# Performance work log

Measured on AMD Instinct MI355X. Metric: run time of the kernel, lower is better.

Reference implementation:

```python
import jax, jax.numpy as jnp
import numpy as np

B, T, V, D, P, DEP = 64, 32, 32000, 1024, 8, 4
TAU = 1.0
EPS = 1e-5


def setup_inputs() -> dict:
    key = jax.random.key(0)
    ks = jax.random.split(key, 9)
    s = 0.02
    x = jax.random.randint(ks[0], (B, T), 0, V)
    emb = jax.random.normal(ks[1], (V, D), jnp.float32) * s
    pos = jax.random.normal(ks[2], (T, D), jnp.float32) * s
    # primitive library: n_prims MLPs (Linear -> GELU -> Linear), stacked
    w1 = jax.random.normal(ks[3], (P, D, D), jnp.float32) * s
    b1 = jnp.zeros((P, D), jnp.float32)
    w2 = jax.random.normal(ks[4], (P, D, D), jnp.float32) * s
    b2 = jnp.zeros((P, D), jnp.float32)
    # one selector Linear(dim, n_prims) per depth
    sel_w = jax.random.normal(ks[5], (DEP, P, D), jnp.float32) * s
    sel_b = jnp.zeros((DEP, P), jnp.float32)
    ln_g = jnp.ones((D,), jnp.float32)
    ln_b = jnp.zeros((D,), jnp.float32)
    head_w = jax.random.normal(ks[6], (V, D), jnp.float32) * s
    # fixed gumbel noise (replaces torch's in-op sampling, kept deterministic)
    u = jax.random.uniform(ks[7], (DEP, B, P), jnp.float32, 1e-6, 1.0 - 1e-6)
    gumbel = -jnp.log(-jnp.log(u))
    return dict(x=x, emb=emb, pos=pos, w1=w1, b1=b1, w2=w2, b2=b2,
                sel_w=sel_w, sel_b=sel_b, ln_g=ln_g, ln_b=ln_b,
                head_w=head_w, gumbel=gumbel)


def reference(x, emb, pos, w1, b1, w2, b2, sel_w, sel_b, ln_g, ln_b, head_w, gumbel):
    h = emb[x] + pos[None, :x.shape[1], :]          # [B,T,D]
    div = jnp.float32(0.0)
    unif = jnp.float32(1.0 / P)
    for d in range(DEP):
        ctx = h.mean(axis=1)                         # [B,D]
        logits = ctx @ sel_w[d].T + sel_b[d]         # [B,P]
        weights = jax.nn.softmax((logits + gumbel[d]) / TAU, axis=-1)
        # all primitives over all tokens at once (grouped GEMM), no T loop
        u1 = jax.nn.gelu(jnp.einsum('btd,pde->btpe', h, w1) + b1, approximate=False)
        prim = jnp.einsum('btpe,pef->btpf', u1, w2) + b2   # [B,T,P,D]
        h = h + jnp.einsum('btpf,bp->btf', prim, weights)  # residual add
        avg = weights.mean(axis=0)                   # [P]
        # F.kl_div(avg.log(), uniform, reduction='sum')
        div = div + jnp.sum(unif * (jnp.log(unif) - jnp.log(avg)))
    mu = h.mean(-1, keepdims=True)
    var = ((h - mu) ** 2).mean(-1, keepdims=True)
    hn = (h - mu) * jax.lax.rsqrt(var + EPS) * ln_g + ln_b
    return hn @ head_w.T, div
```

## Files before the change

kernel.cpp:

```cpp
#include <hip/hip_runtime.h>
#include <hip/hip_bf16.h>
#include <math.h>

typedef __bf16 bf16x8 __attribute__((ext_vector_type(8)));
typedef float  f32x4  __attribute__((ext_vector_type(4)));

struct __align__(8) bf16x4s { __hip_bfloat16 a, b, c, d; };

__device__ __forceinline__ void gload_lds16(const void* g, void* l) {
  __builtin_amdgcn_global_load_lds(
      (const __attribute__((address_space(1))) void*)g,
      (__attribute__((address_space(3))) void*)l, 16, 0, 0);
}

__device__ __forceinline__ float fast_gelu(float v) {
  float s = 0.70710678118654752f * v;
  float a = fabsf(s);
  float t = __builtin_amdgcn_rcpf(fmaf(0.3275911f, a, 1.0f));
  float p = t * fmaf(t, fmaf(t, fmaf(t, fmaf(t, 1.061405429f, -1.453152027f),
                                     1.421413741f), -0.284496736f), 0.254829592f);
  float e = __expf(-a * a);
  float er = copysignf(fmaf(-p, e, 1.0f), s);
  return 0.5f * v * (1.0f + er);
}

#define BAR()   asm volatile("s_barrier" ::: "memory")
#define SB0()   __builtin_amdgcn_sched_barrier(0)
#define VMC(N)  do { asm volatile("s_waitcnt vmcnt(" #N ")" ::: "memory"); \
                     __builtin_amdgcn_sched_barrier(0); } while (0)
#define P1()    __builtin_amdgcn_s_setprio(1)
#define P0()    __builtin_amdgcn_s_setprio(0)

#define MQ(MB, NB, AV, BV)                                                    \
  do {                                                                        \
    _Pragma("unroll")                                                         \
    for (int mi_ = 0; mi_ < 4; ++mi_)                                         \
      _Pragma("unroll")                                                       \
      for (int nj_ = 0; nj_ < 2; ++nj_)                                       \
        _Pragma("unroll")                                                     \
        for (int kk_ = 0; kk_ < 2; ++kk_)                                     \
          acc[MB + mi_][NB + nj_] = __builtin_amdgcn_mfma_f32_16x16x32_bf16(  \
              AV[mi_][kk_], BV[nj_][kk_], acc[MB + mi_][NB + nj_], 0, 0, 0);  \
  } while (0)

template<int EPI>
__global__ __launch_bounds__(512, 2)
void gemm_nt(const __hip_bfloat16* __restrict__ A,
             const __hip_bfloat16* __restrict__ B,
             const int K, const int Kc, const int N,
             const float* __restrict__ p0,
             const float* __restrict__ p1,
             float* __restrict__ f32out,
             __hip_bfloat16* __restrict__ bfout)
{
  __shared__ __align__(16) __hip_bfloat16 lds[65536];

  const int tid = threadIdx.x;
  const int lane = tid & 63, wid = tid >> 6;
  const int l15 = lane & 15, l4 = lane >> 4;
  const int r8 = lane >> 3, blk = lane & 7;
  const int wm = wid >> 2, wn = wid & 3;

  const int nx = gridDim.x;
  const int flat = blockIdx.x + nx * blockIdx.y;
  const int q = (nx * gridDim.y) >> 3;
  const int nid = (flat & 7) * q + (flat >> 3);
  const long m0 = (long)(nid % nx) * 256;
  const long n0 = (long)(nid / nx) * 256;

  const int kbeg = blockIdx.z * Kc;
  const int nt = Kc / 64;

  f32x4 acc[8][4] = {};
  bf16x8 arE[4][2], arL[4][2], brE[2][2], brL[2][2];

  auto stageA = [&](int buf, int h, int k0) {
#pragma unroll
    for (int p2 = 0; p2 < 2; ++p2) {
      int ch = p2 * 16 + h * 8 + wid;
      int row = ch * 8 + r8;
      gload_lds16(A + (m0 + row) * (long)K + k0 + ((blk ^ r8) << 3),
                  lds + buf * 16384 + ch * 512);
    }
  };
  auto stageB = [&](int buf, int h, int k0) {
#pragma unroll
    for (int p2 = 0; p2 < 2; ++p2) {
      int ch = (p2 * 2 + (wid >> 2)) * 8 + h * 4 + (wid & 3);
      int row = ch * 8 + r8;
      gload_lds16(B + (n0 + row) * (long)K + k0 + ((blk ^ r8) << 3),
                  lds + 32768 + buf * 16384 + ch * 512);
    }
  };
  auto readAE = [&](int buf) {
    const __hip_bfloat16* pA = lds + buf * 16384;
#pragma unroll
    for (int mi = 0; mi < 4; ++mi)
#pragma unroll
      for (int kk = 0; kk < 2; ++kk) {
        int row = wm * 128 + mi * 16 + l15;
        arE[mi][kk] = *(const bf16x8*)(pA + row * 64 + (((kk * 4 + l4) ^ (row & 7)) << 3));
      }
  };
  auto readAL = [&](int buf) {
    const __hip_bfloat16* pA = lds + buf * 16384;
#pragma unroll
    for (int mi = 0; mi < 4; ++mi)
#pragma unroll
      for (int kk = 0; kk < 2; ++kk) {
        int row = wm * 128 + 64 + mi * 16 + l15;
        arL[mi][kk] = *(const bf16x8*)(pA + row * 64 + (((kk * 4 + l4) ^ (row & 7)) << 3));
      }
  };
  auto readBE = [&](int buf) {
    const __hip_bfloat16* pB = lds + 32768 + buf * 16384;
#pragma unroll
    for (int nj = 0; nj < 2; ++nj)
#pragma unroll
      for (int kk = 0; kk < 2; ++kk) {
        int row = wn * 64 + nj * 16 + l15;
        brE[nj][kk] = *(const bf16x8*)(pB + row * 64 + (((kk * 4 + l4) ^ (row & 7)) << 3));
      }
  };
  auto readBL = [&](int buf) {
    const __hip_bfloat16* pB = lds + 32768 + buf * 16384;
#pragma unroll
    for (int nj = 0; nj < 2; ++nj)
#pragma unroll
      for (int kk = 0; kk < 2; ++kk) {
        int row = wn * 64 + 32 + nj * 16 + l15;
        brL[nj][kk] = *(const bf16x8*)(pB + row * 64 + (((kk * 4 + l4) ^ (row & 7)) << 3));
      }
  };

  stageA(0, 0, kbeg);
  stageB(0, 0, kbeg);
  stageB(0, 1, kbeg);
  stageA(0, 1, kbeg);
  stageA(1, 0, kbeg + 64);
  stageB(1, 0, kbeg + 64);
  stageB(1, 1, kbeg + 64);
  VMC(8);
  BAR();
  readAE(0); readBE(0);

  for (int s = 0; s < nt - 2; ++s) {
    const int b = s & 1;
    const int k1 = kbeg + (s + 1) * 64, k2 = kbeg + (s + 2) * 64;
    readBL(b);
    stageA(b ^ 1, 1, k1);
    SB0();
    P1(); MQ(0, 0, arE, brE); P0();
    VMC(8); BAR();
    readAL(b);
    stageA(b, 0, k2);
    SB0();
    P1(); MQ(0, 2, arE, brL); P0();
    VMC(8); BAR();
    readAE(b ^ 1);
    stageB(b, 0, k2);
    SB0();
    P1(); MQ(4, 0, arL, brE); P0();
    VMC(8); BAR();
    readBE(b ^ 1);
    stageB(b, 1, k2);
    SB0();
    P1(); MQ(4, 2, arL, brL); P0();
    VMC(8); BAR();
  }

  {
    const int b = (nt - 2) & 1;
    readBL(b);
    stageA(b ^ 1, 1, kbeg + (nt - 1) * 64);
    SB0();
    P1(); MQ(0, 0, arE, brE); P0();
    VMC(8); BAR();
    readAL(b);
    SB0();
    P1(); MQ(0, 2, arE, brL); P0();
    VMC(6); BAR();
    readAE(b ^ 1);
    SB0();
    P1(); MQ(4, 0, arL, brE); P0();
    VMC(4); BAR();
    readBE(b ^ 1);
    SB0();
    P1(); MQ(4, 2, arL, brL); P0();
    VMC(2); BAR();
  }
  {
    const int b = (nt - 1) & 1;
    readBL(b);
    SB0();
    P1(); MQ(0, 0, arE, brE); P0();
    VMC(0); BAR();
    readAL(b);
    SB0();
    P1(); MQ(0, 2, arE, brL); P0();
    P1(); MQ(4, 0, arL, brE); P0();
    P1(); MQ(4, 2, arL, brL); P0();
  }

  const long slab = (EPI == 2) ? (long)blockIdx.z * (long)(gridDim.x * 256) * N : 0;
#pragma unroll
  for (int mi = 0; mi < 8; ++mi) {
    const long gmb = m0 + wm * 128 + mi * 16 + l4 * 4;
    const int b = (int)(gmb >> 5);
#pragma unroll
    for (int nj = 0; nj < 4; ++nj) {
      const long gn = n0 + wn * 64 + nj * 16 + l15;
      if constexpr (EPI == 0) {
        const int p = (int)(gn >> 10), e = (int)(gn & 1023);
        const float bias = p0[(p << 10) + e];
        const float wpb = p1[(b << 3) + p];
#pragma unroll
        for (int r = 0; r < 4; ++r) {
          float v = fast_gelu(acc[mi][nj][r] + bias) * wpb;
          bfout[(gmb + r) * (long)N + gn] = __float2bfloat16(v);
        }
      } else if constexpr (EPI == 2) {
#pragma unroll
        for (int r = 0; r < 4; ++r)
          f32out[slab + (gmb + r) * (long)N + gn] = acc[mi][nj][r];
      } else {
#pragma unroll
        for (int r = 0; r < 4; ++r)
          __builtin_nontemporal_store(acc[mi][nj][r], f32out + (gmb + r) * (long)N + gn);
      }
    }
  }
}

__global__ void cvt_bf16_k(const float* __restrict__ in, __hip_bfloat16* __restrict__ out, long n) {
  long i = ((long)blockIdx.x * blockDim.x + threadIdx.x) * 4;
  if (i >= n) return;
  float4 v = *(const float4*)(in + i);
  *(bf16x4s*)(out + i) = bf16x4s{__float2bfloat16(v.x), __float2bfloat16(v.y),
                                 __float2bfloat16(v.z), __float2bfloat16(v.w)};
}

__global__ void tconv_k(const float* __restrict__ in, __hip_bfloat16* __restrict__ out,
                        long in_bs, long out_rs, long out_bs) {
  __shared__ float tile[32][33];
  int p = blockIdx.z;
  int r0 = blockIdx.y * 32, c0 = blockIdx.x * 32;
  int tx = threadIdx.x, ty = threadIdx.y;
#pragma unroll
  for (int i = 0; i < 32; i += 8)
    tile[ty + i][tx] = in[(long)p * in_bs + (long)(r0 + ty + i) * 1024 + c0 + tx];
  __syncthreads();
#pragma unroll
  for (int i = 0; i < 32; i += 8)
    out[(long)(c0 + ty + i) * out_rs + (long)p * out_bs + (r0 + tx)] =
        __float2bfloat16(tile[tx][ty + i]);
}

__global__ void embed_k(const int* __restrict__ x, const float* __restrict__ emb,
                        const float* __restrict__ pos, float* __restrict__ h,
                        __hip_bfloat16* __restrict__ hb, float* __restrict__ divp) {
  int row = blockIdx.x;
  int t = row & 31;
  int c = threadIdx.x * 4;
  long tok = x[row];
  float4 e = *(const float4*)(emb + tok * 1024 + c);
  float4 q = *(const float4*)(pos + (long)t * 1024 + c);
  float4 v{e.x + q.x, e.y + q.y, e.z + q.z, e.w + q.w};
  *(float4*)(h + (long)row * 1024 + c) = v;
  *(bf16x4s*)(hb + (long)row * 1024 + c) =
      bf16x4s{__float2bfloat16(v.x), __float2bfloat16(v.y),
              __float2bfloat16(v.z), __float2bfloat16(v.w)};
  if (row == 0 && threadIdx.x == 0) *divp = 0.f;
}

__global__ void select_wb2_k(const float* __restrict__ h, const float* __restrict__ selw,
                             const float* __restrict__ selb, const float* __restrict__ gum,
                             const float* __restrict__ b2, float* __restrict__ W,
                             float* __restrict__ wb2, int dep) {
  int b = blockIdx.x, tid = threadIdx.x;
  int c = tid * 4;
  float4 s{0.f, 0.f, 0.f, 0.f};
  for (int t = 0; t < 32; ++t) {
    const float4 v = *(const float4*)(h + ((long)(b * 32 + t)) * 1024 + c);
    s.x += v.x; s.y += v.y; s.z += v.z; s.w += v.w;
  }
  float lp[8];
#pragma unroll
  for (int p = 0; p < 8; ++p) {
    const float4 w = *(const float4*)(selw + dep * 8192 + p * 1024 + c);
    lp[p] = (s.x * w.x + s.y * w.y + s.z * w.z + s.w * w.w) * (1.f / 32.f);
  }
  int lane = tid & 63, wid = tid >> 6;
#pragma unroll
  for (int p = 0; p < 8; ++p)
    for (int o = 32; o; o >>= 1) lp[p] += __shfl_down(lp[p], o);
  __shared__ float red[4][8];
  __shared__ float wsm[8];
  if (lane == 0) {
#pragma unroll
    for (int p = 0; p < 8; ++p) red[wid][p] = lp[p];
  }
  __syncthreads();
  if (tid == 0) {
    float lg[8], mx = -1e30f;
    for (int p = 0; p < 8; ++p) {
      lg[p] = red[0][p] + red[1][p] + red[2][p] + red[3][p]
            + selb[dep * 8 + p] + gum[dep * 512 + b * 8 + p];
      mx = fmaxf(mx, lg[p]);
    }
    float sm = 0.f;
    for (int p = 0; p < 8; ++p) { lg[p] = expf(lg[p] - mx); sm += lg[p]; }
    float inv = 1.f / sm;
    for (int p = 0; p < 8; ++p) { wsm[p] = lg[p] * inv; W[dep * 512 + b * 8 + p] = lg[p] * inv; }
  }
  __syncthreads();
  float4 a{0.f, 0.f, 0.f, 0.f};
#pragma unroll
  for (int p = 0; p < 8; ++p) {
    float wp = wsm[p];
    const float4 v = *(const float4*)(b2 + p * 1024 + c);
    a.x += wp * v.x; a.y += wp * v.y; a.z += wp * v.z; a.w += wp * v.w;
  }
  *(float4*)(wb2 + (long)b * 1024 + c) = a;
}

__global__ void h_update_k(const float* __restrict__ part, float* __restrict__ h,
                           const float* __restrict__ wb2, __hip_bfloat16* __restrict__ hb,
                           const float* __restrict__ Wd, float* __restrict__ divp) {
  int row = blockIdx.x;
  int c = threadIdx.x * 4;
  long idx = (long)row * 1024 + c;
  float4 a = *(const float4*)(h + idx);
  const float4 w = *(const float4*)(wb2 + (long)(row >> 5) * 1024 + c);
  a.x += w.x; a.y += w.y; a.z += w.z; a.w += w.w;
#pragma unroll
  for (int s = 0; s < 8; ++s) {
    const float4 v = *(const float4*)(part + (long)s * 2097152 + idx);
    a.x += v.x; a.y += v.y; a.z += v.z; a.w += v.w;
  }
  *(float4*)(h + idx) = a;
  *(bf16x4s*)(hb + idx) = bf16x4s{__float2bfloat16(a.x), __float2bfloat16(a.y),
                                  __float2bfloat16(a.z), __float2bfloat16(a.w)};
  if (blockIdx.x == 0 && threadIdx.x < 64) {
    float w8[8];
#pragma unroll
    for (int p = 0; p < 8; ++p) w8[p] = Wd[threadIdx.x * 8 + p];
#pragma unroll
    for (int p = 0; p < 8; ++p)
      for (int o = 32; o; o >>= 1) w8[p] += __shfl_down(w8[p], o);
    if (threadIdx.x == 0) {
      float d = *divp;
      const float u = 0.125f, lu = logf(0.125f);
#pragma unroll
      for (int p = 0; p < 8; ++p) d += u * (lu - logf(w8[p] * (1.f / 64.f)));
      *divp = d;
    }
  }
}

__global__ void ln_k(const float* __restrict__ h, const float* __restrict__ g,
                     const float* __restrict__ be, __hip_bfloat16* __restrict__ hnb,
                     const float* __restrict__ divp, float* __restrict__ divout) {
  int row = blockIdx.x, tid = threadIdx.x;
  int c = tid * 4;
  const float4 v = *(const float4*)(h + (long)row * 1024 + c);
  float s = v.x + v.y + v.z + v.w;
  float q = v.x * v.x + v.y * v.y + v.z * v.z + v.w * v.w;
  for (int o = 32; o; o >>= 1) { s += __shfl_down(s, o); q += __shfl_down(q, o); }
  __shared__ float red[16];
  int lane = tid & 63, wid = tid >> 6;
  if (lane == 0) { red[wid] = s; red[8 + wid] = q; }
  __syncthreads();
  if (tid == 0) {
    float S = red[0] + red[1] + red[2] + red[3];
    float Q = red[8] + red[9] + red[10] + red[11];
    float mu = S * (1.f / 1024.f);
    float var = Q * (1.f / 1024.f) - mu * mu;
    red[0] = mu; red[1] = rsqrtf(var + 1e-5f);
  }
  __syncthreads();
  float mu = red[0], rs = red[1];
  float4 gg = *(const float4*)(g + c), bb = *(const float4*)(be + c);
  *(bf16x4s*)(hnb + (long)row * 1024 + c) =
      bf16x4s{__float2bfloat16((v.x - mu) * rs * gg.x + bb.x),
              __float2bfloat16((v.y - mu) * rs * gg.y + bb.y),
              __float2bfloat16((v.z - mu) * rs * gg.z + bb.z),
              __float2bfloat16((v.w - mu) * rs * gg.w + bb.w)};
  if (row == 0 && tid == 0) *divout = *divp;
}

extern "C" void kernel_launch(void* const* d_in, const int* in_sizes, int n_in,
                              void* d_out, int out_size, void* d_ws, size_t ws_size,
                              hipStream_t stream) {
  (void)in_sizes; (void)n_in; (void)out_size; (void)ws_size;
  const int*   x     = (const int*)  d_in[0];
  const float* emb   = (const float*)d_in[1];
  const float* pos   = (const float*)d_in[2];
  const float* w1    = (const float*)d_in[3];
  const float* b1    = (const float*)d_in[4];
  const float* w2    = (const float*)d_in[5];
  const float* b2    = (const float*)d_in[6];
  const float* selw  = (const float*)d_in[7];
  const float* selb  = (const float*)d_in[8];
  const float* lng   = (const float*)d_in[9];
  const float* lnb   = (const float*)d_in[10];
  const float* headw = (const float*)d_in[11];
  const float* gum   = (const float*)d_in[12];
  float* out = (float*)d_out;

  char* ws = (char*)d_ws;
  __hip_bfloat16* w1t   = (__hip_bfloat16*)(ws);
  __hip_bfloat16* w2t   = (__hip_bfloat16*)(ws + 16777216);
  __hip_bfloat16* headb = (__hip_bfloat16*)(ws + 33554432);
  float*          h     = (float*)(ws + 99090432);
  __hip_bfloat16* hb    = (__hip_bfloat16*)(ws + 107479040);
  __hip_bfloat16* u1    = (__hip_bfloat16*)(ws + 111673344);
  float*          Wall  = (float*)(ws + 145227776);
  float*          wb2   = (float*)(ws + 145240064);
  float*          divp  = (float*)(ws + 145502208);
  float*          part  = out;

  cvt_bf16_k<<<32000, 256, 0, stream>>>(headw, headb, 32768000L);
  tconv_k<<<dim3(32, 32, 8), dim3(32, 8), 0, stream>>>(w1, w1t, 1L << 20, 1024L, 1L << 20);
  tconv_k<<<dim3(32, 32, 8), dim3(32, 8), 0, stream>>>(w2, w2t, 1L << 20, 8192L, 1024L);
  embed_k<<<2048, 256, 0, stream>>>(x, emb, pos, h, hb, divp);

  for (int d = 0; d < 4; ++d) {
    select_wb2_k<<<64, 256, 0, stream>>>(h, selw, selb, gum, b2, Wall, wb2, d);
    gemm_nt<0><<<dim3(8, 32), 512, 0, stream>>>(hb, w1t, 1024, 1024, 8192, b1, Wall + d * 512, nullptr, u1);
    gemm_nt<2><<<dim3(8, 4, 8), 512, 0, stream>>>(u1, w2t, 8192, 1024, 1024, nullptr, nullptr, part, nullptr);
    h_update_k<<<2048, 256, 0, stream>>>(part, h, wb2, hb, Wall + d * 512, divp);
  }

  ln_k<<<2048, 256, 0, stream>>>(h, lng, lnb, hb, divp, out + 65536000L);
  gemm_nt<3><<<dim3(8, 125), 512, 0, stream>>>(hb, headb, 1024, 1024, 32000, nullptr, nullptr, out, nullptr);
}
```

Before: 697.7 us.

## Simplify GEMM main loop to per-tile double buffering and drop nontemporal head stores

Replaces the finely interleaved four-phase GEMM loop, which staged quarter tiles between MFMA groups, with a simpler loop. Each iteration reads the remaining LDS fragments, issues all 32 MFMAs, waits on LDS, barriers, then issues the whole next-next tile load and barriers again. The head GEMM also switches from nontemporal stores to regular stores through the EPI==2 path, with slab zero because gridDim.z is 1. The goal is less scheduling and barrier overhead per phase, but global loads now overlap compute less finely and each iteration has two full barriers.

```diff
diff --git a/kernel.cpp b/kernel.cpp
--- a/kernel.cpp
+++ b/kernel.cpp
@@ -25,7 +25,8 @@
 }
 
 #define BAR()   asm volatile("s_barrier" ::: "memory")
-#define SB0()   __builtin_amdgcn_sched_barrier(0)
+#define LGKM0() do { asm volatile("s_waitcnt lgkmcnt(0)" ::: "memory"); \
+                     __builtin_amdgcn_sched_barrier(0); } while (0)
 #define VMC(N)  do { asm volatile("s_waitcnt vmcnt(" #N ")" ::: "memory"); \
                      __builtin_amdgcn_sched_barrier(0); } while (0)
 #define P1()    __builtin_amdgcn_s_setprio(1)
@@ -92,6 +93,10 @@
                   lds + 32768 + buf * 16384 + ch * 512);
     }
   };
+  auto stage4 = [&](int buf, int k0) {
+    stageA(buf, 0, k0); stageA(buf, 1, k0);
+    stageB(buf, 0, k0); stageB(buf, 1, k0);
+  };
   auto readAE = [&](int buf) {
     const __hip_bfloat16* pA = lds + buf * 16384;
 #pragma unroll
@@ -133,73 +138,31 @@
       }
   };
 
-  stageA(0, 0, kbeg);
-  stageB(0, 0, kbeg);
-  stageB(0, 1, kbeg);
-  stageA(0, 1, kbeg);
-  stageA(1, 0, kbeg + 64);
-  stageB(1, 0, kbeg + 64);
-  stageB(1, 1, kbeg + 64);
+  stage4(0, kbeg);
+  stage4(1, kbeg + 64);
   VMC(8);
   BAR();
   readAE(0); readBE(0);
 
-  for (int s = 0; s < nt - 2; ++s) {
+  for (int s = 0; s < nt; ++s) {
     const int b = s & 1;
-    const int k1 = kbeg + (s + 1) * 64, k2 = kbeg + (s + 2) * 64;
-    readBL(b);
-    stageA(b ^ 1, 1, k1);
-    SB0();
-    P1(); MQ(0, 0, arE, brE); P0();
-    VMC(8); BAR();
-    readAL(b);
-    stageA(b, 0, k2);
-    SB0();
-    P1(); MQ(0, 2, arE, brL); P0();
-    VMC(8); BAR();
-    readAE(b ^ 1);
-    stageB(b, 0, k2);
-    SB0();
-    P1(); MQ(4, 0, arL, brE); P0();
-    VMC(8); BAR();
-    readBE(b ^ 1);
-    stageB(b, 1, k2);
-    SB0();
-    P1(); MQ(4, 2, arL, brL); P0();
-    VMC(8); BAR();
-  }
-
-  {
-    const int b = (nt - 2) & 1;
-    readBL(b);
-    stageA(b ^ 1, 1, kbeg + (nt - 1) * 64);
-    SB0();
-    P1(); MQ(0, 0, arE, brE); P0();
-    VMC(8); BAR();
-    readAL(b);
-    SB0();
-    P1(); MQ(0, 2, arE, brL); P0();
-    VMC(6); BAR();
-    readAE(b ^ 1);
-    SB0();
-    P1(); MQ(4, 0, arL, brE); P0();
-    VMC(4); BAR();
-    readBE(b ^ 1);
-    SB0();
-    P1(); MQ(4, 2, arL, brL); P0();
-    VMC(2); BAR();
-  }
-  {
-    const int b = (nt - 1) & 1;
-    readBL(b);
-    SB0();
-    P1(); MQ(0, 0, arE, brE); P0();
-    VMC(0); BAR();
-    readAL(b);
-    SB0();
-    P1(); MQ(0, 2, arE, brL); P0();
-    P1(); MQ(4, 0, arL, brE); P0();
-    P1(); MQ(4, 2, arL, brL); P0();
+    readBL(b); readAL(b);
+    P1();
+    MQ(0, 0, arE, brE);
+    MQ(0, 2, arE, brL);
+    MQ(4, 0, arL, brE);
+    MQ(4, 2, arL, brL);
+    P0();
+    LGKM0();
+    BAR();
+    if (s + 2 < nt) {
+      stage4(b, kbeg + (s + 2) * 64);
+      VMC(8);
+    } else if (s + 2 == nt) {
+      VMC(0);
+    }
+    BAR();
+    if (s + 1 < nt) { readAE(b ^ 1); readBE(b ^ 1); }
   }
 
   const long slab = (EPI == 2) ? (long)blockIdx.z * (long)(gridDim.x * 256) * N : 0;
@@ -219,14 +182,10 @@
           float v = fast_gelu(acc[mi][nj][r] + bias) * wpb;
           bfout[(gmb + r) * (long)N + gn] = __float2bfloat16(v);
         }
-      } else if constexpr (EPI == 2) {
+      } else {
 #pragma unroll
         for (int r = 0; r < 4; ++r)
           f32out[slab + (gmb + r) * (long)N + gn] = acc[mi][nj][r];
-      } else {
-#pragma unroll
-        for (int r = 0; r < 4; ++r)
-          __builtin_nontemporal_store(acc[mi][nj][r], f32out + (gmb + r) * (long)N + gn);
       }
     }
   }
@@ -433,5 +392,5 @@
   }
 
   ln_k<<<2048, 256, 0, stream>>>(h, lng, lnb, hb, divp, out + 65536000L);
-  gemm_nt<3><<<dim3(8, 125), 512, 0, stream>>>(hb, headb, 1024, 1024, 32000, nullptr, nullptr, out, nullptr);
-}
+  gemm_nt<2><<<dim3(8, 125), 512, 0, stream>>>(hb, headb, 1024, 1024, 32000, nullptr, nullptr, out, nullptr);
+}
```

Result: faster. 662.8 us (-5.0%).
